# Optimization experiments

Hardware: AMD Instinct MI355X
Metric: run time of the kernel (lower is better)

## Reference

```python
import jax, jax.numpy as jnp
import numpy as np

B, N, D, K, E = 64, 512, 16, 16, 128
LN_EPS = 1e-5


def _layernorm(h, g, b):
    m = jnp.mean(h, axis=-1, keepdims=True)
    v = jnp.mean(jnp.square(h - m), axis=-1, keepdims=True)
    return (h - m) * jax.lax.rsqrt(v + LN_EPS) * g + b


def _linear_init(key, fan_in, fan_out):
    s = 1.0 / np.sqrt(fan_in)
    kw, kb = jax.random.split(key)
    W = jax.random.uniform(kw, (fan_in, fan_out), jnp.float32, -s, s)
    b = jax.random.uniform(kb, (fan_out,), jnp.float32, -s, s)
    return W, b


def setup_inputs() -> dict:
    key = jax.random.key(0)
    ks = jax.random.split(key, 4)
    x = jax.random.normal(ks[0], (B, N, D), jnp.float32)
    W1, b1 = _linear_init(ks[1], 2 * D, E)
    W2, b2 = _linear_init(ks[2], E, E)
    W3, b3 = _linear_init(ks[3], E, E)
    ones, zeros = jnp.ones((E,), jnp.float32), jnp.zeros((E,), jnp.float32)
    return {
        "x": x,
        "W1": W1, "b1": b1, "g1": ones, "be1": zeros,
        "W2": W2, "b2": b2, "g2": ones, "be2": zeros,
        "W3": W3, "b3": b3, "g3": ones, "be3": zeros,
    }


def reference(x, W1, b1, g1, be1, W2, b2, g2, be2, W3, b3, g3, be3):
    # kNN on coordinate features (columns 8, 9)
    xy = x[..., 8:10]                                   # [B, N, 2]
    d2 = jnp.sum(jnp.square(xy[:, :, None, :] - xy[:, None, :, :]), axis=-1)  # [B, N, N]
    _, idx = jax.lax.top_k(-d2, K)                      # smallest distances -> [B, N, K]

    # gather neighbor features per batch
    neighbors = jax.vmap(lambda xb, ib: xb[ib])(x, idx)  # [B, N, K, D]
    central = jnp.broadcast_to(x[:, :, None, :], (B, N, K, D))
    feats = jnp.concatenate([central, neighbors - central], axis=-1)  # [B, N, K, 2D]

    h = jax.nn.gelu(_layernorm(feats @ W1 + b1, g1, be1), approximate=False)
    h = jax.nn.gelu(_layernorm(h @ W2 + b2, g2, be2), approximate=False)
    h = jax.nn.gelu(_layernorm(h @ W3 + b3, g3, be3), approximate=False)  # [B, N, K, E]

    return jnp.mean(h, axis=2)                          # [B, N, E]
```

## Files before the change

kernel.cpp:

```cpp
#include <hip/hip_runtime.h>
#include <math.h>

#define Bdim 64
#define Ndim 512
#define Ddim 16
#define Kdim 16
#define Edim 128
#define LN_EPS 1e-5f

#define PTS   2
#define NT    8
#define KS2   4

typedef __attribute__((ext_vector_type(8))) short bf16x8;
typedef __attribute__((ext_vector_type(4))) float f32x4;
typedef __attribute__((ext_vector_type(2))) float f32x2;

#if __has_builtin(__builtin_amdgcn_exp2f)
#define EXP2F __builtin_amdgcn_exp2f
#else
#define EXP2F exp2f
#endif

template<int CTRL>
__device__ __forceinline__ unsigned dpp_u32(unsigned v) {
    return (unsigned)__builtin_amdgcn_update_dpp(0, (int)v, CTRL, 0xF, 0xF, true);
}
template<int CTRL>
__device__ __forceinline__ unsigned dpp_u32_keep(unsigned v) {
    return (unsigned)__builtin_amdgcn_update_dpp((int)v, (int)v, CTRL, 0xF, 0xF, false);
}
template<int CTRL>
__device__ __forceinline__ float dpp_f32(float v) {
    return __int_as_float(__builtin_amdgcn_update_dpp(0, __float_as_int(v), CTRL, 0xF, 0xF, true));
}
__device__ __forceinline__ unsigned min_u32(unsigned a, unsigned b) { return (b < a) ? b : a; }

__device__ __forceinline__ unsigned short f2bf(float f) {
    unsigned u = __float_as_uint(f);
    unsigned r = (u + 0x7FFFu + ((u >> 16) & 1u)) >> 16;
    return (unsigned short)r;
}

__device__ __forceinline__ unsigned cvt_pk_bf16(float a, float b) {
    unsigned r;
    asm("v_cvt_pk_bf16_f32 %0, %1, %2" : "=v"(r) : "v"(a), "v"(b));
    return r;
}

__device__ __forceinline__ f32x2 gelu2(f32x2 x) {
    f32x2 x2 = x * x;
    f32x2 t  = x2 * (f32x2){-0.10294324f, -0.10294324f}
                  + (f32x2){-2.30220821f, -2.30220821f};
    f32x2 z  = x * t;
    f32x2 e  = { EXP2F(z.x), EXP2F(z.y) };
    f32x2 d  = e + (f32x2){1.0f, 1.0f};
    f32x2 r  = { __builtin_amdgcn_rcpf(d.x), __builtin_amdgcn_rcpf(d.y) };
    return x * r;
}

__global__ __launch_bounds__(256) void pack_w_kernel(
    const float* __restrict__ W1, const float* __restrict__ W2,
    const float* __restrict__ W3,
    const float* __restrict__ g1, const float* __restrict__ be1,
    const float* __restrict__ g2, const float* __restrict__ be2,
    const float* __restrict__ g3, const float* __restrict__ be3,
    unsigned short* __restrict__ wp)
{
    int idx = blockIdx.x * 256 + threadIdx.x;
    if (idx >= 37632) return;
    if (idx < 4096) {
        int t = idx;
        int nt = t >> 9, l = (t >> 3) & 63, j = t & 7;
        int k = 8 * (l >> 4) + j, n = nt * 16 + (l & 15);
        wp[idx] = f2bf(W1[k * Edim + n]);
    } else if (idx < 20480) {
        int t = idx - 4096;
        int nt = t >> 11, ks = (t >> 9) & 3, l = (t >> 3) & 63, j = t & 7;
        int k = ks * 32 + 8 * (l >> 4) + j, n = nt * 16 + (l & 15);
        wp[idx] = f2bf(W2[k * Edim + n]);
    } else if (idx < 36864) {
        int t = idx - 20480;
        int nt = t >> 11, ks = (t >> 9) & 3, l = (t >> 3) & 63, j = t & 7;
        int k = ks * 32 + 8 * (l >> 4) + j, n = nt * 16 + (l & 15);
        wp[idx] = f2bf(W3[k * Edim + n]);
    } else {
        int t = idx - 36864;
        int lay = t >> 8;
        int e   = t & 255;
        int nt  = e >> 5;
        int cl  = (e >> 1) & 15;
        int comp = e & 1;
        const float* g  = (lay == 0) ? g1  : (lay == 1) ? g2  : g3;
        const float* be = (lay == 0) ? be1 : (lay == 1) ? be2 : be3;
        float v = comp ? be[nt*16 + cl] : g[nt*16 + cl];
        ((float*)wp)[18432 + t] = v;
    }
}

__device__ __forceinline__ void ln_gelu_acc(
    f32x4 acc[NT], const float2* __restrict__ gbeL, int lane)
{
    const int cl = lane & 15;
    f32x2 s01 = {0.f,0.f}, s23 = {0.f,0.f}, q01 = {0.f,0.f}, q23 = {0.f,0.f};
    #pragma unroll
    for (int nt = 0; nt < NT; ++nt) {
        f32x2 a01 = { acc[nt][0], acc[nt][1] };
        f32x2 a23 = { acc[nt][2], acc[nt][3] };
        s01 += a01;  q01 += a01 * a01;
        s23 += a23;  q23 += a23 * a23;
    }
    #define ROTSTEP(C) {                                                     \
        f32x2 t_;                                                            \
        t_.x = dpp_f32<C>(s01.x); t_.y = dpp_f32<C>(s01.y); s01 += t_;       \
        t_.x = dpp_f32<C>(s23.x); t_.y = dpp_f32<C>(s23.y); s23 += t_;       \
        t_.x = dpp_f32<C>(q01.x); t_.y = dpp_f32<C>(q01.y); q01 += t_;       \
        t_.x = dpp_f32<C>(q23.x); t_.y = dpp_f32<C>(q23.y); q23 += t_;       \
    }
    ROTSTEP(0x121) ROTSTEP(0x122) ROTSTEP(0x124) ROTSTEP(0x128)
    #undef ROTSTEP

    const f32x2 inv128 = { 1.0f/128.0f, 1.0f/128.0f };
    f32x2 m01 = s01 * inv128, m23 = s23 * inv128;
    f32x2 v01 = q01 * inv128 - m01 * m01;
    f32x2 v23 = q23 * inv128 - m23 * m23;
    f32x2 r01 = { __builtin_amdgcn_rsqf(v01.x + LN_EPS), __builtin_amdgcn_rsqf(v01.y + LN_EPS) };
    f32x2 r23 = { __builtin_amdgcn_rsqf(v23.x + LN_EPS), __builtin_amdgcn_rsqf(v23.y + LN_EPS) };

    #pragma unroll
    for (int nt = 0; nt < NT; ++nt) {
        const float2 gb = gbeL[nt*16 + cl];
        const f32x2 gg = { gb.x, gb.x }, bb = { gb.y, gb.y };
        f32x2 a01 = { acc[nt][0], acc[nt][1] };
        f32x2 a23 = { acc[nt][2], acc[nt][3] };
        f32x2 w01 = (a01 - m01) * r01;
        f32x2 w23 = (a23 - m23) * r23;
        w01 = w01 * gg + bb;
        w23 = w23 * gg + bb;
        w01 = gelu2(w01);
        w23 = gelu2(w23);
        acc[nt][0] = w01.x; acc[nt][1] = w01.y;
        acc[nt][2] = w23.x; acc[nt][3] = w23.y;
    }
}

__device__ __forceinline__ void store_h(
    const f32x4 acc[NT], unsigned short* __restrict__ s_h, int wave, int lane)
{
    const int cl = lane & 15, gq = lane >> 4;
    const int rbase = 16*wave + 4*gq;
    #pragma unroll
    for (int nt = 0; nt < NT; ++nt) {
        const int col = nt*16 + cl;
        const int cb  = col >> 3;
        const unsigned r01 = cvt_pk_bf16(acc[nt][0], acc[nt][1]);
        const unsigned r23 = cvt_pk_bf16(acc[nt][2], acc[nt][3]);
        const int a0 = (rbase+0)*128 + ((cb ^ ((rbase+0) & 7)) << 3) + (col & 7);
        const int a1 = (rbase+1)*128 + ((cb ^ ((rbase+1) & 7)) << 3) + (col & 7);
        const int a2 = (rbase+2)*128 + ((cb ^ ((rbase+2) & 7)) << 3) + (col & 7);
        const int a3 = (rbase+3)*128 + ((cb ^ ((rbase+3) & 7)) << 3) + (col & 7);
        s_h[a0] = (unsigned short)(r01 & 0xFFFFu);
        s_h[a1] = (unsigned short)(r01 >> 16);
        s_h[a2] = (unsigned short)(r23 & 0xFFFFu);
        s_h[a3] = (unsigned short)(r23 >> 16);
    }
}

__global__ __launch_bounds__(128, 5) void edgeconv_mfma(
    const float* __restrict__ x,
    const unsigned short* __restrict__ wp,
    const float* __restrict__ b1, const float* __restrict__ b2,
    const float* __restrict__ b3,
    float* __restrict__ out)
{
    const int tid  = threadIdx.x;
    const int wave = tid >> 6, lane = tid & 63;
    const int bp = blockIdx.x;
    const int b  = bp >> 8;
    const int n0 = (bp & 255) * PTS;
    const int n  = n0 + wave;

    __shared__ __align__(16) unsigned short s_h[32 * 128];

    const float* __restrict__ xb = x + (size_t)b * (Ndim * Ddim);
    const float2* __restrict__ gbep = (const float2*)((const float*)wp + 18432);
    const int cl = lane & 15, gq = lane >> 4;

    unsigned my_nb = 0;
    {
        const float qx = xb[n * Ddim + 8], qy = xb[n * Ddim + 9];
        unsigned long long key[8];
        #pragma unroll
        for (int c = 0; c < 8; ++c) {
            int j = c * 64 + lane;
            const float2 p2 = *(const float2*)(xb + j * Ddim + 8);
            float dx = __fsub_rn(qx, p2.x);
            float dy = __fsub_rn(qy, p2.y);
            float d2 = __fadd_rn(__fmul_rn(dx,dx), __fmul_rn(dy,dy));
            key[c] = ((unsigned long long)__float_as_uint(d2) << 32) | (unsigned)j;
        }
        #define CE(A,B) { bool c_ = key[A] < key[B];                          \
                          unsigned long long lo_ = c_ ? key[A] : key[B];      \
                          unsigned long long hi_ = c_ ? key[B] : key[A];      \
                          key[A] = lo_; key[B] = hi_; }
        CE(0,1) CE(2,3) CE(4,5) CE(6,7)
        CE(0,2) CE(1,3) CE(4,6) CE(5,7)
        CE(1,2) CE(5,6)
        CE(0,4) CE(1,5) CE(2,6) CE(3,7)
        CE(2,4) CE(3,5)
        CE(1,2) CE(3,4) CE(5,6)
        #undef CE

        unsigned d2h[8], idxh[8];
        #pragma unroll
        for (int c = 0; c < 8; ++c) {
            d2h[c]  = (unsigned)(key[c] >> 32);
            idxh[c] = (unsigned)key[c];
        }

        #pragma unroll
        for (int sel = 0; sel < Kdim; ++sel) {
            unsigned m = d2h[0];
            m = min_u32(m, dpp_u32<0x121>(m));
            m = min_u32(m, dpp_u32<0x122>(m));
            m = min_u32(m, dpp_u32<0x124>(m));
            m = min_u32(m, dpp_u32<0x128>(m));
            m = min_u32(m, dpp_u32_keep<0x142>(m));
            m = min_u32(m, dpp_u32_keep<0x143>(m));
            const unsigned gmin = (unsigned)__builtin_amdgcn_readlane((int)m, 63);

            const unsigned long long tied = __ballot(d2h[0] == gmin);
            unsigned widx;
            if (__popcll(tied) == 1) {
                const int s = (int)(__ffsll((long long)tied) - 1);
                widx = (unsigned)__builtin_amdgcn_readlane((int)idxh[0], s);
            } else {
                unsigned t = (d2h[0] == gmin) ? idxh[0] : 0xFFFFFFFFu;
                t = min_u32(t, dpp_u32<0x121>(t));
                t = min_u32(t, dpp_u32<0x122>(t));
                t = min_u32(t, dpp_u32<0x124>(t));
                t = min_u32(t, dpp_u32<0x128>(t));
                t = min_u32(t, dpp_u32_keep<0x142>(t));
                t = min_u32(t, dpp_u32_keep<0x143>(t));
                widx = (unsigned)__builtin_amdgcn_readlane((int)t, 63);
            }
            if ((lane & 15) == sel) my_nb = widx;
            if (sel < Kdim - 1) {
                if (d2h[0] == gmin && idxh[0] == widx) {
                    d2h[0]=d2h[1]; d2h[1]=d2h[2]; d2h[2]=d2h[3]; d2h[3]=d2h[4];
                    d2h[4]=d2h[5]; d2h[5]=d2h[6]; d2h[6]=d2h[7]; d2h[7]=0xFFFFFFFFu;
                    idxh[0]=idxh[1]; idxh[1]=idxh[2]; idxh[2]=idxh[3]; idxh[3]=idxh[4];
                    idxh[4]=idxh[5]; idxh[5]=idxh[6]; idxh[6]=idxh[7];
                }
            }
        }
    }

    f32x4 acc[NT];

    {
        const int off8 = (gq & 1) * 8;
        const float* pc = xb + n * Ddim + off8;
        const float* pn = xb + (int)my_nb * Ddim + off8;
        float4 c0 = *(const float4*)(pc);
        float4 c1 = *(const float4*)(pc + 4);
        float4 v0 = *(const float4*)(pn);
        float4 v1 = *(const float4*)(pn + 4);
        const bool diff = (gq >= 2);
        float e0 = diff ? (v0.x - c0.x) : c0.x;
        float e1 = diff ? (v0.y - c0.y) : c0.y;
        float e2 = diff ? (v0.z - c0.z) : c0.z;
        float e3 = diff ? (v0.w - c0.w) : c0.w;
        float e4 = diff ? (v1.x - c1.x) : c1.x;
        float e5 = diff ? (v1.y - c1.y) : c1.y;
        float e6 = diff ? (v1.z - c1.z) : c1.z;
        float e7 = diff ? (v1.w - c1.w) : c1.w;
        union { unsigned u[4]; bf16x8 v; } a1u;
        a1u.u[0] = cvt_pk_bf16(e0, e1);
        a1u.u[1] = cvt_pk_bf16(e2, e3);
        a1u.u[2] = cvt_pk_bf16(e4, e5);
        a1u.u[3] = cvt_pk_bf16(e6, e7);
        const bf16x8 a1 = a1u.v;

        #pragma unroll
        for (int nt = 0; nt < NT; ++nt) {
            const float bv = b1[nt*16 + cl];
            bf16x8 bfr = *(const bf16x8*)(wp + (nt*64 + lane)*8);
            f32x4 c = {bv, bv, bv, bv};
            acc[nt] = __builtin_amdgcn_mfma_f32_16x16x32_bf16(a1, bfr, c, 0, 0, 0);
        }
    }
    ln_gelu_acc(acc, gbep, lane);
    store_h(acc, s_h, wave, lane);

    #pragma unroll 1
    for (int layer = 0; layer < 2; ++layer) {
        const unsigned short* wpL = wp + (layer == 0 ? 4096 : 20480);
        const float* bL = (layer == 0) ? b2 : b3;
        const float2* gbeL = gbep + (layer == 0 ? 128 : 256);

        bf16x8 a[KS2];
        {
            const int row = 16*wave + cl;
            #pragma unroll
            for (int ks = 0; ks < KS2; ++ks) {
                const int cb = ks*4 + gq;
                a[ks] = *(const bf16x8*)(&s_h[row*128 + ((cb ^ (row & 7)) << 3)]);
            }
        }
        #pragma unroll
        for (int nt = 0; nt < NT; ++nt) {
            const float bv = bL[nt*16 + cl];
            f32x4 c = {bv, bv, bv, bv};
            #pragma unroll
            for (int ks = 0; ks < KS2; ++ks) {
                bf16x8 bfr = *(const bf16x8*)(wpL + ((nt*KS2 + ks)*64 + lane)*8);
                c = __builtin_amdgcn_mfma_f32_16x16x32_bf16(a[ks], bfr, c, 0, 0, 0);
            }
            acc[nt] = c;
        }
        ln_gelu_acc(acc, gbeL, lane);
        if (layer == 0) store_h(acc, s_h, wave, lane);
    }

    #pragma unroll
    for (int nt = 0; nt < NT; ++nt) {
        f32x2 p = { acc[nt][0], acc[nt][1] };
        f32x2 q = { acc[nt][2], acc[nt][3] };
        f32x2 h = p + q;
        float sv = h.x + h.y;
        sv += __shfl_xor(sv, 16, 64);
        sv += __shfl_xor(sv, 32, 64);
        if (gq == (nt >> 1))
            out[((size_t)b * Ndim + n) * Edim + nt*16 + cl] = sv * (1.0f/16.0f);
    }
}

extern "C" void kernel_launch(void* const* d_in, const int* in_sizes, int n_in,
                              void* d_out, int out_size, void* d_ws, size_t ws_size,
                              hipStream_t stream)
{
    const float* x   = (const float*)d_in[0];
    const float* W1  = (const float*)d_in[1];
    const float* b1  = (const float*)d_in[2];
    const float* g1  = (const float*)d_in[3];
    const float* be1 = (const float*)d_in[4];
    const float* W2  = (const float*)d_in[5];
    const float* b2  = (const float*)d_in[6];
    const float* g2  = (const float*)d_in[7];
    const float* be2 = (const float*)d_in[8];
    const float* W3  = (const float*)d_in[9];
    const float* b3  = (const float*)d_in[10];
    const float* g3  = (const float*)d_in[11];
    const float* be3 = (const float*)d_in[12];
    float* out = (float*)d_out;
    unsigned short* wp = (unsigned short*)d_ws;

    hipLaunchKernelGGL(pack_w_kernel, dim3(147), dim3(256), 0, stream,
                       W1, W2, W3, g1, be1, g2, be2, g3, be3, wp);
    hipLaunchKernelGGL(edgeconv_mfma, dim3((Bdim * Ndim) / PTS), dim3(128), 0, stream,
                       x, wp, b1, b2, b3, out);
}
```

Before: 174.3 us.

## Process two query points per wave to reuse weight fragments and interleave kNN

```diff
diff --git a/kernel.cpp b/kernel.cpp
--- a/kernel.cpp
+++ b/kernel.cpp
@@ -8,7 +8,7 @@
 #define Edim 128
 #define LN_EPS 1e-5f
 
-#define PTS   2
+#define PTS   4
 #define NT    8
 #define KS2   4
 
@@ -98,8 +98,40 @@
     }
 }
 
+__device__ __forceinline__ void knn_round(
+    unsigned (&d2h)[8], unsigned (&idxh)[8], unsigned &my_nb, int sel, int lane, bool pop)
+{
+    unsigned m = d2h[0];
+    m = min_u32(m, dpp_u32<0x121>(m));
+    m = min_u32(m, dpp_u32<0x122>(m));
+    m = min_u32(m, dpp_u32<0x124>(m));
+    m = min_u32(m, dpp_u32<0x128>(m));
+    m = min_u32(m, dpp_u32_keep<0x142>(m));
+    m = min_u32(m, dpp_u32_keep<0x143>(m));
+    const unsigned gmin = (unsigned)__builtin_amdgcn_readlane((int)m, 63);
+
+    unsigned t = (d2h[0] == gmin) ? idxh[0] : 0xFFFFFFFFu;
+    t = min_u32(t, dpp_u32<0x121>(t));
+    t = min_u32(t, dpp_u32<0x122>(t));
+    t = min_u32(t, dpp_u32<0x124>(t));
+    t = min_u32(t, dpp_u32<0x128>(t));
+    t = min_u32(t, dpp_u32_keep<0x142>(t));
+    t = min_u32(t, dpp_u32_keep<0x143>(t));
+    const unsigned widx = (unsigned)__builtin_amdgcn_readlane((int)t, 63);
+
+    if ((lane & 15) == sel) my_nb = widx;
+    if (pop) {
+        if (d2h[0] == gmin && idxh[0] == widx) {
+            d2h[0]=d2h[1]; d2h[1]=d2h[2]; d2h[2]=d2h[3]; d2h[3]=d2h[4];
+            d2h[4]=d2h[5]; d2h[5]=d2h[6]; d2h[6]=d2h[7]; d2h[7]=0xFFFFFFFFu;
+            idxh[0]=idxh[1]; idxh[1]=idxh[2]; idxh[2]=idxh[3]; idxh[3]=idxh[4];
+            idxh[4]=idxh[5]; idxh[5]=idxh[6]; idxh[6]=idxh[7];
+        }
+    }
+}
+
 __device__ __forceinline__ void ln_gelu_acc(
-    f32x4 acc[NT], const float2* __restrict__ gbeL, int lane)
+    f32x4 (&acc)[NT], const float2* __restrict__ gbeL, int lane)
 {
     const int cl = lane & 15;
     f32x2 s01 = {0.f,0.f}, s23 = {0.f,0.f}, q01 = {0.f,0.f}, q23 = {0.f,0.f};
@@ -145,10 +177,10 @@
 }
 
 __device__ __forceinline__ void store_h(
-    const f32x4 acc[NT], unsigned short* __restrict__ s_h, int wave, int lane)
+    const f32x4 (&acc)[NT], unsigned short* __restrict__ s_h, int rbase0, int lane)
 {
     const int cl = lane & 15, gq = lane >> 4;
-    const int rbase = 16*wave + 4*gq;
+    const int rbase = rbase0 + 4*gq;
     #pragma unroll
     for (int nt = 0; nt < NT; ++nt) {
         const int col = nt*16 + cl;
@@ -166,7 +198,7 @@
     }
 }
 
-__global__ __launch_bounds__(128, 5) void edgeconv_mfma(
+__global__ __launch_bounds__(128, 3) void edgeconv_mfma(
     const float* __restrict__ x,
     const unsigned short* __restrict__ wp,
     const float* __restrict__ b1, const float* __restrict__ b2,
@@ -176,122 +208,105 @@
     const int tid  = threadIdx.x;
     const int wave = tid >> 6, lane = tid & 63;
     const int bp = blockIdx.x;
-    const int b  = bp >> 8;
-    const int n0 = (bp & 255) * PTS;
-    const int n  = n0 + wave;
-
-    __shared__ __align__(16) unsigned short s_h[32 * 128];
+    const int b  = bp >> 7;
+    const int n0 = (bp & 127) * PTS;
+    const int nA = n0 + 2*wave;
+    const int nB = nA + 1;
+
+    __shared__ __align__(16) unsigned short s_h[64 * 128];
 
     const float* __restrict__ xb = x + (size_t)b * (Ndim * Ddim);
     const float2* __restrict__ gbep = (const float2*)((const float*)wp + 18432);
     const int cl = lane & 15, gq = lane >> 4;
 
-    unsigned my_nb = 0;
+    unsigned my_nbA = 0, my_nbB = 0;
+    unsigned d2A[8], ixA[8], d2B[8], ixB[8];
     {
-        const float qx = xb[n * Ddim + 8], qy = xb[n * Ddim + 9];
-        unsigned long long key[8];
+        const float qxA = xb[nA * Ddim + 8], qyA = xb[nA * Ddim + 9];
+        const float qxB = xb[nB * Ddim + 8], qyB = xb[nB * Ddim + 9];
+        unsigned long long keyA[8], keyB[8];
         #pragma unroll
         for (int c = 0; c < 8; ++c) {
             int j = c * 64 + lane;
             const float2 p2 = *(const float2*)(xb + j * Ddim + 8);
-            float dx = __fsub_rn(qx, p2.x);
-            float dy = __fsub_rn(qy, p2.y);
-            float d2 = __fadd_rn(__fmul_rn(dx,dx), __fmul_rn(dy,dy));
-            key[c] = ((unsigned long long)__float_as_uint(d2) << 32) | (unsigned)j;
-        }
-        #define CE(A,B) { bool c_ = key[A] < key[B];                          \
-                          unsigned long long lo_ = c_ ? key[A] : key[B];      \
-                          unsigned long long hi_ = c_ ? key[B] : key[A];      \
-                          key[A] = lo_; key[B] = hi_; }
-        CE(0,1) CE(2,3) CE(4,5) CE(6,7)
-        CE(0,2) CE(1,3) CE(4,6) CE(5,7)
-        CE(1,2) CE(5,6)
-        CE(0,4) CE(1,5) CE(2,6) CE(3,7)
-        CE(2,4) CE(3,5)
-        CE(1,2) CE(3,4) CE(5,6)
+            float dxA = __fsub_rn(qxA, p2.x), dyA = __fsub_rn(qyA, p2.y);
+            float dxB = __fsub_rn(qxB, p2.x), dyB = __fsub_rn(qyB, p2.y);
+            float dA = __fadd_rn(__fmul_rn(dxA,dxA), __fmul_rn(dyA,dyA));
+            float dB = __fadd_rn(__fmul_rn(dxB,dxB), __fmul_rn(dyB,dyB));
+            keyA[c] = ((unsigned long long)__float_as_uint(dA) << 32) | (unsigned)j;
+            keyB[c] = ((unsigned long long)__float_as_uint(dB) << 32) | (unsigned)j;
+        }
+        #define CE(K,A,B) { bool c_ = K[A] < K[B];                            \
+                            unsigned long long lo_ = c_ ? K[A] : K[B];        \
+                            unsigned long long hi_ = c_ ? K[B] : K[A];        \
+                            K[A] = lo_; K[B] = hi_; }
+        #define SORT8(K) CE(K,0,1) CE(K,2,3) CE(K,4,5) CE(K,6,7)              \
+                         CE(K,0,2) CE(K,1,3) CE(K,4,6) CE(K,5,7)              \
+                         CE(K,1,2) CE(K,5,6)                                  \
+                         CE(K,0,4) CE(K,1,5) CE(K,2,6) CE(K,3,7)              \
+                         CE(K,2,4) CE(K,3,5)                                  \
+                         CE(K,1,2) CE(K,3,4) CE(K,5,6)
+        SORT8(keyA)
+        SORT8(keyB)
+        #undef SORT8
         #undef CE
-
-        unsigned d2h[8], idxh[8];
         #pragma unroll
         for (int c = 0; c < 8; ++c) {
-            d2h[c]  = (unsigned)(key[c] >> 32);
-            idxh[c] = (unsigned)key[c];
-        }
-
-        #pragma unroll
-        for (int sel = 0; sel < Kdim; ++sel) {
-            unsigned m = d2h[0];
-            m = min_u32(m, dpp_u32<0x121>(m));
-            m = min_u32(m, dpp_u32<0x122>(m));
-            m = min_u32(m, dpp_u32<0x124>(m));
-            m = min_u32(m, dpp_u32<0x128>(m));
-            m = min_u32(m, dpp_u32_keep<0x142>(m));
-            m = min_u32(m, dpp_u32_keep<0x143>(m));
-            const unsigned gmin = (unsigned)__builtin_amdgcn_readlane((int)m, 63);
-
-            const unsigned long long tied = __ballot(d2h[0] == gmin);
-            unsigned widx;
-            if (__popcll(tied) == 1) {
-                const int s = (int)(__ffsll((long long)tied) - 1);
-                widx = (unsigned)__builtin_amdgcn_readlane((int)idxh[0], s);
-            } else {
-                unsigned t = (d2h[0] == gmin) ? idxh[0] : 0xFFFFFFFFu;
-                t = min_u32(t, dpp_u32<0x121>(t));
-                t = min_u32(t, dpp_u32<0x122>(t));
-                t = min_u32(t, dpp_u32<0x124>(t));
-                t = min_u32(t, dpp_u32<0x128>(t));
-                t = min_u32(t, dpp_u32_keep<0x142>(t));
-                t = min_u32(t, dpp_u32_keep<0x143>(t));
-                widx = (unsigned)__builtin_amdgcn_readlane((int)t, 63);
-            }
-            if ((lane & 15) == sel) my_nb = widx;
-            if (sel < Kdim - 1) {
-                if (d2h[0] == gmin && idxh[0] == widx) {
-                    d2h[0]=d2h[1]; d2h[1]=d2h[2]; d2h[2]=d2h[3]; d2h[3]=d2h[4];
-                    d2h[4]=d2h[5]; d2h[5]=d2h[6]; d2h[6]=d2h[7]; d2h[7]=0xFFFFFFFFu;
-                    idxh[0]=idxh[1]; idxh[1]=idxh[2]; idxh[2]=idxh[3]; idxh[3]=idxh[4];
-                    idxh[4]=idxh[5]; idxh[5]=idxh[6]; idxh[6]=idxh[7];
-                }
-            }
-        }
-    }
-
-    f32x4 acc[NT];
+            d2A[c] = (unsigned)(keyA[c] >> 32);  ixA[c] = (unsigned)keyA[c];
+            d2B[c] = (unsigned)(keyB[c] >> 32);  ixB[c] = (unsigned)keyB[c];
+        }
+    }
+    #pragma unroll
+    for (int sel = 0; sel < Kdim; ++sel) {
+        const bool pop = (sel < Kdim - 1);
+        knn_round(d2A, ixA, my_nbA, sel, lane, pop);
+        knn_round(d2B, ixB, my_nbB, sel, lane, pop);
+    }
+
+    f32x4 acc[2][NT];
 
     {
         const int off8 = (gq & 1) * 8;
-        const float* pc = xb + n * Ddim + off8;
-        const float* pn = xb + (int)my_nb * Ddim + off8;
-        float4 c0 = *(const float4*)(pc);
-        float4 c1 = *(const float4*)(pc + 4);
-        float4 v0 = *(const float4*)(pn);
-        float4 v1 = *(const float4*)(pn + 4);
         const bool diff = (gq >= 2);
-        float e0 = diff ? (v0.x - c0.x) : c0.x;
-        float e1 = diff ? (v0.y - c0.y) : c0.y;
-        float e2 = diff ? (v0.z - c0.z) : c0.z;
-        float e3 = diff ? (v0.w - c0.w) : c0.w;
-        float e4 = diff ? (v1.x - c1.x) : c1.x;
-        float e5 = diff ? (v1.y - c1.y) : c1.y;
-        float e6 = diff ? (v1.z - c1.z) : c1.z;
-        float e7 = diff ? (v1.w - c1.w) : c1.w;
-        union { unsigned u[4]; bf16x8 v; } a1u;
-        a1u.u[0] = cvt_pk_bf16(e0, e1);
-        a1u.u[1] = cvt_pk_bf16(e2, e3);
-        a1u.u[2] = cvt_pk_bf16(e4, e5);
-        a1u.u[3] = cvt_pk_bf16(e6, e7);
-        const bf16x8 a1 = a1u.v;
-
+        bf16x8 a1[2];
+        #pragma unroll
+        for (int mt = 0; mt < 2; ++mt) {
+            const int n = (mt == 0) ? nA : nB;
+            const unsigned nb = (mt == 0) ? my_nbA : my_nbB;
+            const float* pc = xb + n * Ddim + off8;
+            const float* pn = xb + (int)nb * Ddim + off8;
+            float4 c0 = *(const float4*)(pc);
+            float4 c1 = *(const float4*)(pc + 4);
+            float4 v0 = *(const float4*)(pn);
+            float4 v1 = *(const float4*)(pn + 4);
+            float e0 = diff ? (v0.x - c0.x) : c0.x;
+            float e1 = diff ? (v0.y - c0.y) : c0.y;
+            float e2 = diff ? (v0.z - c0.z) : c0.z;
+            float e3 = diff ? (v0.w - c0.w) : c0.w;
+            float e4 = diff ? (v1.x - c1.x) : c1.x;
+            float e5 = diff ? (v1.y - c1.y) : c1.y;
+            float e6 = diff ? (v1.z - c1.z) : c1.z;
+            float e7 = diff ? (v1.w - c1.w) : c1.w;
+            union { unsigned u[4]; bf16x8 v; } a1u;
+            a1u.u[0] = cvt_pk_bf16(e0, e1);
+            a1u.u[1] = cvt_pk_bf16(e2, e3);
+            a1u.u[2] = cvt_pk_bf16(e4, e5);
+            a1u.u[3] = cvt_pk_bf16(e6, e7);
+            a1[mt] = a1u.v;
+        }
         #pragma unroll
         for (int nt = 0; nt < NT; ++nt) {
             const float bv = b1[nt*16 + cl];
             bf16x8 bfr = *(const bf16x8*)(wp + (nt*64 + lane)*8);
             f32x4 c = {bv, bv, bv, bv};
-            acc[nt] = __builtin_amdgcn_mfma_f32_16x16x32_bf16(a1, bfr, c, 0, 0, 0);
-        }
-    }
-    ln_gelu_acc(acc, gbep, lane);
-    store_h(acc, s_h, wave, lane);
+            acc[0][nt] = __builtin_amdgcn_mfma_f32_16x16x32_bf16(a1[0], bfr, c, 0, 0, 0);
+            acc[1][nt] = __builtin_amdgcn_mfma_f32_16x16x32_bf16(a1[1], bfr, c, 0, 0, 0);
+        }
+    }
+    ln_gelu_acc(acc[0], gbep, lane);
+    ln_gelu_acc(acc[1], gbep, lane);
+    store_h(acc[0], s_h, 32*wave +  0, lane);
+    store_h(acc[1], s_h, 32*wave + 16, lane);
 
     #pragma unroll 1
     for (int layer = 0; layer < 2; ++layer) {
@@ -299,40 +314,54 @@
         const float* bL = (layer == 0) ? b2 : b3;
         const float2* gbeL = gbep + (layer == 0 ? 128 : 256);
 
-        bf16x8 a[KS2];
-        {
-            const int row = 16*wave + cl;
+        bf16x8 a[2][KS2];
+        #pragma unroll
+        for (int mt = 0; mt < 2; ++mt) {
+            const int row = 32*wave + 16*mt + cl;
             #pragma unroll
             for (int ks = 0; ks < KS2; ++ks) {
                 const int cb = ks*4 + gq;
-                a[ks] = *(const bf16x8*)(&s_h[row*128 + ((cb ^ (row & 7)) << 3)]);
+                a[mt][ks] = *(const bf16x8*)(&s_h[row*128 + ((cb ^ (row & 7)) << 3)]);
             }
         }
         #pragma unroll
         for (int nt = 0; nt < NT; ++nt) {
             const float bv = bL[nt*16 + cl];
-            f32x4 c = {bv, bv, bv, bv};
+            bf16x8 bfr[KS2];
             #pragma unroll
-            for (int ks = 0; ks < KS2; ++ks) {
-                bf16x8 bfr = *(const bf16x8*)(wpL + ((nt*KS2 + ks)*64 + lane)*8);
-                c = __builtin_amdgcn_mfma_f32_16x16x32_bf16(a[ks], bfr, c, 0, 0, 0);
+            for (int ks = 0; ks < KS2; ++ks)
+                bfr[ks] = *(const bf16x8*)(wpL + ((nt*KS2 + ks)*64 + lane)*8);
+            #pragma unroll
+            for (int mt = 0; mt < 2; ++mt) {
+                f32x4 c = {bv, bv, bv, bv};
+                #pragma unroll
+                for (int ks = 0; ks < KS2; ++ks)
+                    c = __builtin_amdgcn_mfma_f32_16x16x32_bf16(a[mt][ks], bfr[ks], c, 0, 0, 0);
+                acc[mt][nt] = c;
             }
-            acc[nt] = c;
-        }
-        ln_gelu_acc(acc, gbeL, lane);
-        if (layer == 0) store_h(acc, s_h, wave, lane);
-    }
-
-    #pragma unroll
-    for (int nt = 0; nt < NT; ++nt) {
-        f32x2 p = { acc[nt][0], acc[nt][1] };
-        f32x2 q = { acc[nt][2], acc[nt][3] };
-        f32x2 h = p + q;
-        float sv = h.x + h.y;
-        sv += __shfl_xor(sv, 16, 64);
-        sv += __shfl_xor(sv, 32, 64);
-        if (gq == (nt >> 1))
-            out[((size_t)b * Ndim + n) * Edim + nt*16 + cl] = sv * (1.0f/16.0f);
+        }
+        ln_gelu_acc(acc[0], gbeL, lane);
+        ln_gelu_acc(acc[1], gbeL, lane);
+        if (layer == 0) {
+            store_h(acc[0], s_h, 32*wave +  0, lane);
+            store_h(acc[1], s_h, 32*wave + 16, lane);
+        }
+    }
+
+    #pragma unroll
+    for (int mt = 0; mt < 2; ++mt) {
+        const int n = (mt == 0) ? nA : nB;
+        #pragma unroll
+        for (int nt = 0; nt < NT; ++nt) {
+            f32x2 p = { acc[mt][nt][0], acc[mt][nt][1] };
+            f32x2 q = { acc[mt][nt][2], acc[mt][nt][3] };
+            f32x2 h = p + q;
+            float sv = h.x + h.y;
+            sv += __shfl_xor(sv, 16, 64);
+            sv += __shfl_xor(sv, 32, 64);
+            if (gq == (nt >> 1))
+                out[((size_t)b * Ndim + n) * Edim + nt*16 + cl] = sv * (1.0f/16.0f);
+        }
     }
 }
 
```

New measurement: 163.6 us. -6.1%, faster.
